# Kernel optimization log

Measured on AMD Instinct MI355X. Metric: run time of the kernel, lower is better.

The kernel has to match this reference:

```python
import jax, jax.numpy as jnp
import numpy as np

KSIZE = 3  # kernel_size from init_kwargs


def _unfold_same(x, ks):
    """Torch nn.Unfold with fixed 'same' padding. x:(B,C,H,W) -> (B, C*ks*ks, H, W).
    Channel ordering matches torch unfold: (c, kh, kw) with c outermost."""
    B, C, H, W = x.shape
    pad_total = ks - 1
    pb = pad_total // 2
    pe = pad_total - pb
    xp = jnp.pad(x, ((0, 0), (0, 0), (pb, pe), (pb, pe)))
    # small fixed loop over ks*ks = 9 taps
    patches = jnp.stack(
        [xp[:, :, di:di + H, dj:dj + W] for di in range(ks) for dj in range(ks)],
        axis=2,
    )  # (B, C, ks*ks, H, W)
    return patches.reshape(B, C * ks * ks, H, W)


def setup_inputs() -> dict:
    key = jax.random.key(0)
    k1, k2 = jax.random.split(key)
    B, C, H, W = 16, 32, 256, 256
    O, ks = 64, KSIZE
    K = C * ks * ks  # 288
    x = jax.random.normal(k1, (B, C, H, W), dtype=jnp.float32)
    limit = float(np.sqrt(6.0 / (K + O)))  # xavier_uniform
    weight = jax.random.uniform(k2, (O, K), jnp.float32, -limit, limit)
    bias = jnp.zeros((O, 1), dtype=jnp.float32)
    return {"x": x, "weight": weight, "bias": bias}


def reference(x, weight, bias):
    # Faithful math of Linear.forward: same-padded unfold, then per-pixel
    # out[n,o] = sum_k weight[o,k] * patch[n,k] + bias[o], reshaped to (B,O,H,W).
    # Expressed as a single contraction instead of the (N,O,K) broadcast intermediate.
    patches = _unfold_same(x, KSIZE)                     # (B, K, H, W)
    out = jnp.einsum('ok,bkhw->bohw', weight, patches)   # (B, O, H, W)
    out = out + bias.reshape(1, -1, 1, 1)
    return out
```

## Files before the change

kernel.cpp:

```cpp
#include <hip/hip_runtime.h>
#include <hip/hip_bf16.h>

#define CIN 32
#define OCH 64
#define HH  256
#define WW  256
#define HW  (HH * WW)
#define BH  8
#define ROWB (258 * CIN * 2)

typedef __bf16 bf16x8 __attribute__((ext_vector_type(8)));
typedef float  f32x4  __attribute__((ext_vector_type(4)));

__global__ __launch_bounds__(256, 2) void conv_fused_kernel(
        const float* __restrict__ x, const float* __restrict__ wgt,
        const float* __restrict__ bias, float* __restrict__ out) {
    const int bid = blockIdx.x;
    const int nid = (bid & 7) * 64 + (bid >> 3);
    const int b   = nid >> 5;
    const int h0  = (nid & 31) * BH;
    const int tid = threadIdx.x;
    const int l   = tid & 63, wid = tid >> 6;
    const int lm  = l & 15,  lh  = l >> 4;

    __shared__ __bf16 xs[4][258][CIN];
    char* lds = (char*)&xs[0][0][0];
    const float* xb = x + (size_t)b * CIN * HW;

    if (tid < 32) {
        const int s = tid >> 3, k = tid & 7;
        const int wp = (k < 4) ? 0 : 257;
        *(f32x4*)(lds + s * ROWB + wp * 64 + (k & 3) * 16) = (f32x4){0, 0, 0, 0};
    }

    bf16x8 af[9];
    {
        const float* wp_ = wgt + (size_t)(wid * 16 + lm) * 288 + (size_t)lh * 8 * 9;
#pragma unroll
        for (int t = 0; t < 9; ++t)
#pragma unroll
            for (int j = 0; j < 8; ++j)
                af[t][j] = (__bf16)wp_[j * 9 + t];
    }
    float bv[4];
#pragma unroll
    for (int r = 0; r < 4; ++r) bv[r] = bias[wid * 16 + lh * 4 + r];

    auto stage = [&](int row) {
        char* slot = lds + ((row + 1) & 3) * ROWB;
        if (row >= 0 && row < HH) {
            const float* rp = xb + (size_t)row * WW;
#pragma unroll
            for (int wh = 0; wh < 2; ++wh) {
                float2 v[8];
#pragma unroll
                for (int j = 0; j < 8; ++j)
                    v[j] = *(const float2*)(rp + (size_t)(wid * 8 + j) * HW + wh * 128 + 2 * l);
#pragma unroll
                for (int p = 0; p < 2; ++p) {
                    const int w = wh * 128 + 2 * l + p;
                    bf16x8 pk;
#pragma unroll
                    for (int j = 0; j < 8; ++j) pk[j] = (__bf16)(p ? v[j].y : v[j].x);
                    *(bf16x8*)(slot + (w + 1) * 64 + ((wid ^ ((w >> 1) & 3)) << 4)) = pk;
                }
            }
        } else {
#pragma unroll
            for (int wh = 0; wh < 2; ++wh)
#pragma unroll
                for (int p = 0; p < 2; ++p) {
                    const int w = wh * 128 + 2 * l + p;
                    *(f32x4*)(slot + (w + 1) * 64 + ((wid ^ ((w >> 1) & 3)) << 4)) =
                        (f32x4){0, 0, 0, 0};
                }
        }
    };

    stage(h0 - 1); stage(h0); stage(h0 + 1);

    int off[3];
#pragma unroll
    for (int kw = 0; kw < 3; ++kw) {
        const int u = lm + kw - 1;
        const int m = (u < 0) ? 3 : ((u >> 1) & 3);
        off[kw] = (lm + kw) * 64 + ((lh ^ m) << 4);
    }

    __syncthreads();

    for (int i = 0; i < BH; ++i) {
        const int h  = h0 + i;
        const int nr = h + 2;
        const bool ldnext = (i < BH - 1) && (nr < HH);
        const bool zrnext = (i < BH - 1) && (nr >= HH);

        float2 v[16];
        if (ldnext) {
            const float* rp = xb + (size_t)nr * WW;
#pragma unroll
            for (int wh = 0; wh < 2; ++wh)
#pragma unroll
                for (int j = 0; j < 8; ++j)
                    v[wh * 8 + j] =
                        *(const float2*)(rp + (size_t)(wid * 8 + j) * HW + wh * 128 + 2 * l);
        }

        const char* base[3] = { lds + ((h    ) & 3) * ROWB,
                                lds + ((h + 1) & 3) * ROWB,
                                lds + ((h + 2) & 3) * ROWB };
        f32x4 acc[16];
#pragma unroll
        for (int nt = 0; nt < 16; ++nt) acc[nt] = (f32x4){0, 0, 0, 0};
#pragma unroll
        for (int nt = 0; nt < 16; ++nt)
#pragma unroll
            for (int kh = 0; kh < 3; ++kh)
#pragma unroll
                for (int kw = 0; kw < 3; ++kw) {
                    bf16x8 bf = *(const bf16x8*)(base[kh] + off[kw] + nt * 1024);
                    acc[nt] = __builtin_amdgcn_mfma_f32_16x16x32_bf16(
                        af[kh * 3 + kw], bf, acc[nt], 0, 0, 0);
                }

        float* outb = out + (size_t)b * OCH * HW + (size_t)h * WW;
#pragma unroll
        for (int nt = 0; nt < 16; ++nt)
#pragma unroll
            for (int r2 = 0; r2 < 4; ++r2)
                outb[(size_t)(wid * 16 + lh * 4 + r2) * HW + nt * 16 + lm] =
                    acc[nt][r2] + bv[r2];

        if (ldnext) {
            char* slot = lds + ((nr + 1) & 3) * ROWB;
#pragma unroll
            for (int wh = 0; wh < 2; ++wh)
#pragma unroll
                for (int p = 0; p < 2; ++p) {
                    const int w = wh * 128 + 2 * l + p;
                    bf16x8 pk;
#pragma unroll
                    for (int j = 0; j < 8; ++j)
                        pk[j] = (__bf16)(p ? v[wh * 8 + j].y : v[wh * 8 + j].x);
                    *(bf16x8*)(slot + (w + 1) * 64 + ((wid ^ ((w >> 1) & 3)) << 4)) = pk;
                }
        } else if (zrnext) {
            char* slot = lds + ((nr + 1) & 3) * ROWB;
#pragma unroll
            for (int wh = 0; wh < 2; ++wh)
#pragma unroll
                for (int p = 0; p < 2; ++p) {
                    const int w = wh * 128 + 2 * l + p;
                    *(f32x4*)(slot + (w + 1) * 64 + ((wid ^ ((w >> 1) & 3)) << 4)) =
                        (f32x4){0, 0, 0, 0};
                }
        }
        __syncthreads();
    }
}

extern "C" void kernel_launch(void* const* d_in, const int* in_sizes, int n_in,
                              void* d_out, int out_size, void* d_ws, size_t ws_size,
                              hipStream_t stream) {
    const float* x    = (const float*)d_in[0];
    const float* w    = (const float*)d_in[1];
    const float* bias = (const float*)d_in[2];
    float* out = (float*)d_out;

    hipLaunchKernelGGL(conv_fused_kernel, dim3(16 * (HH / BH)), dim3(256), 0, stream,
                       x, w, bias, out);
}
```

Baseline: 109.3 us.

## Split warp work into 2 output groups × 8 pixel tiles to reuse LDS fragments

Each wave now computes two 16-channel output groups over half of the pixel tiles instead of one group over all tiles. Every B fragment read from LDS then feeds two MFMAs, halving LDS reads per MFMA at the cost of holding twice the weight fragments in registers. The bias is folded into the accumulator initialisation, output stores become nontemporal, and the barrier on the last iteration is dropped. The extra weight registers may pressure occupancy under the launch bound of 2 blocks.

```diff
diff --git a/kernel.cpp b/kernel.cpp
--- a/kernel.cpp
+++ b/kernel.cpp
@@ -22,6 +22,8 @@
     const int tid = threadIdx.x;
     const int l   = tid & 63, wid = tid >> 6;
     const int lm  = l & 15,  lh  = l >> 4;
+    const int ogb = (wid & 1) * 2;
+    const int ntb = (wid >> 1) * 8;
 
     __shared__ __bf16 xs[4][258][CIN];
     char* lds = (char*)&xs[0][0][0];
@@ -33,18 +35,22 @@
         *(f32x4*)(lds + s * ROWB + wp * 64 + (k & 3) * 16) = (f32x4){0, 0, 0, 0};
     }
 
-    bf16x8 af[9];
-    {
-        const float* wp_ = wgt + (size_t)(wid * 16 + lm) * 288 + (size_t)lh * 8 * 9;
+    bf16x8 af[2][9];
+#pragma unroll
+    for (int g = 0; g < 2; ++g) {
+        const float* wp_ = wgt + (size_t)((ogb + g) * 16 + lm) * 288 + (size_t)lh * 8 * 9;
 #pragma unroll
         for (int t = 0; t < 9; ++t)
 #pragma unroll
             for (int j = 0; j < 8; ++j)
-                af[t][j] = (__bf16)wp_[j * 9 + t];
+                af[g][t][j] = (__bf16)wp_[j * 9 + t];
     }
-    float bv[4];
+    float bv[2][4];
 #pragma unroll
-    for (int r = 0; r < 4; ++r) bv[r] = bias[wid * 16 + lh * 4 + r];
+    for (int g = 0; g < 2; ++g)
+#pragma unroll
+        for (int r = 0; r < 4; ++r)
+            bv[g][r] = bias[(ogb + g) * 16 + lh * 4 + r];
 
     auto stage = [&](int row) {
         char* slot = lds + ((row + 1) & 3) * ROWB;
@@ -109,27 +115,37 @@
         const char* base[3] = { lds + ((h    ) & 3) * ROWB,
                                 lds + ((h + 1) & 3) * ROWB,
                                 lds + ((h + 2) & 3) * ROWB };
-        f32x4 acc[16];
+        f32x4 acc[8][2];
 #pragma unroll
-        for (int nt = 0; nt < 16; ++nt) acc[nt] = (f32x4){0, 0, 0, 0};
+        for (int nt = 0; nt < 8; ++nt)
 #pragma unroll
-        for (int nt = 0; nt < 16; ++nt)
+            for (int g = 0; g < 2; ++g)
+                acc[nt][g] = (f32x4){bv[g][0], bv[g][1], bv[g][2], bv[g][3]};
+
+#pragma unroll
+        for (int nt = 0; nt < 8; ++nt)
 #pragma unroll
             for (int kh = 0; kh < 3; ++kh)
 #pragma unroll
                 for (int kw = 0; kw < 3; ++kw) {
-                    bf16x8 bf = *(const bf16x8*)(base[kh] + off[kw] + nt * 1024);
-                    acc[nt] = __builtin_amdgcn_mfma_f32_16x16x32_bf16(
-                        af[kh * 3 + kw], bf, acc[nt], 0, 0, 0);
+                    bf16x8 bf = *(const bf16x8*)(base[kh] + off[kw] + (ntb + nt) * 1024);
+                    acc[nt][0] = __builtin_amdgcn_mfma_f32_16x16x32_bf16(
+                        af[0][kh * 3 + kw], bf, acc[nt][0], 0, 0, 0);
+                    acc[nt][1] = __builtin_amdgcn_mfma_f32_16x16x32_bf16(
+                        af[1][kh * 3 + kw], bf, acc[nt][1], 0, 0, 0);
                 }
 
         float* outb = out + (size_t)b * OCH * HW + (size_t)h * WW;
 #pragma unroll
-        for (int nt = 0; nt < 16; ++nt)
+        for (int nt = 0; nt < 8; ++nt)
 #pragma unroll
-            for (int r2 = 0; r2 < 4; ++r2)
-                outb[(size_t)(wid * 16 + lh * 4 + r2) * HW + nt * 16 + lm] =
-                    acc[nt][r2] + bv[r2];
+            for (int g = 0; g < 2; ++g)
+#pragma unroll
+                for (int r2 = 0; r2 < 4; ++r2)
+                    __builtin_nontemporal_store(
+                        acc[nt][g][r2],
+                        &outb[(size_t)((ogb + g) * 16 + lh * 4 + r2) * HW +
+                              (ntb + nt) * 16 + lm]);
 
         if (ldnext) {
             char* slot = lds + ((nr + 1) & 3) * ROWB;
@@ -155,7 +171,7 @@
                         (f32x4){0, 0, 0, 0};
                 }
         }
-        __syncthreads();
+        if (i < BH - 1) __syncthreads();
     }
 }
 
```

Measured after the change: 156.1 us. 42.8% more time.

## Split image width across blocks with halo columns and defer output stores

Applied to the files above, without the earlier changes.

Each block now covers half the image width (128 columns plus two halo columns loaded separately), which doubles the grid to 1024 blocks, halves LDS per block, and raises the launch-bounds occupancy target from 2 to 4. The accumulator count per thread drops from 16 to 8 tiles. Bias is folded into the accumulator initialisation, and the store of each output row is deferred into the next iteration so it can overlap with the following row's loads. In exchange, every input row is loaded with extra halo-column traffic, and the single-element halo loads and stores add scattered accesses.

```diff
diff --git a/kernel.cpp b/kernel.cpp
--- a/kernel.cpp
+++ b/kernel.cpp
@@ -1,37 +1,35 @@
 #include <hip/hip_runtime.h>
 #include <hip/hip_bf16.h>
 
-#define CIN 32
-#define OCH 64
-#define HH  256
-#define WW  256
-#define HW  (HH * WW)
-#define BH  8
-#define ROWB (258 * CIN * 2)
+#define CIN  32
+#define OCH  64
+#define HH   256
+#define WW   256
+#define HW   (HH * WW)
+#define BH   8
+#define NENT 130
+#define ROWB (NENT * 64)
 
 typedef __bf16 bf16x8 __attribute__((ext_vector_type(8)));
 typedef float  f32x4  __attribute__((ext_vector_type(4)));
 
-__global__ __launch_bounds__(256, 2) void conv_fused_kernel(
+__global__ __launch_bounds__(256, 4) void conv_fused_kernel(
         const float* __restrict__ x, const float* __restrict__ wgt,
         const float* __restrict__ bias, float* __restrict__ out) {
     const int bid = blockIdx.x;
-    const int nid = (bid & 7) * 64 + (bid >> 3);
-    const int b   = nid >> 5;
-    const int h0  = (nid & 31) * BH;
+    const int nid = (bid & 7) * 128 + (bid >> 3);
+    const int wh  = nid & 1;
+    const int ht  = (nid >> 1) & 31;
+    const int b   = nid >> 6;
+    const int wbase = wh * 128;
+    const int h0    = ht * BH;
     const int tid = threadIdx.x;
     const int l   = tid & 63, wid = tid >> 6;
     const int lm  = l & 15,  lh  = l >> 4;
 
-    __shared__ __bf16 xs[4][258][CIN];
+    __shared__ __bf16 xs[4][NENT][CIN];
     char* lds = (char*)&xs[0][0][0];
     const float* xb = x + (size_t)b * CIN * HW;
-
-    if (tid < 32) {
-        const int s = tid >> 3, k = tid & 7;
-        const int wp = (k < 4) ? 0 : 257;
-        *(f32x4*)(lds + s * ROWB + wp * 64 + (k & 3) * 16) = (f32x4){0, 0, 0, 0};
-    }
 
     bf16x8 af[9];
     {
@@ -46,116 +44,131 @@
 #pragma unroll
     for (int r = 0; r < 4; ++r) bv[r] = bias[wid * 16 + lh * 4 + r];
 
-    auto stage = [&](int row) {
+    auto stageFull = [&](int row) {
         char* slot = lds + ((row + 1) & 3) * ROWB;
-        if (row >= 0 && row < HH) {
-            const float* rp = xb + (size_t)row * WW;
+        const bool rok = (row >= 0) && (row < HH);
+        const float* rp = xb + (size_t)row * WW;
+        float2 v[8];
 #pragma unroll
-            for (int wh = 0; wh < 2; ++wh) {
-                float2 v[8];
+        for (int j = 0; j < 8; ++j)
+            v[j] = rok ? *(const float2*)(rp + (size_t)(wid * 8 + j) * HW + wbase + 2 * l)
+                       : make_float2(0.f, 0.f);
 #pragma unroll
-                for (int j = 0; j < 8; ++j)
-                    v[j] = *(const float2*)(rp + (size_t)(wid * 8 + j) * HW + wh * 128 + 2 * l);
+        for (int p = 0; p < 2; ++p) {
+            const int w = wbase + 2 * l + p;
+            bf16x8 pk;
 #pragma unroll
-                for (int p = 0; p < 2; ++p) {
-                    const int w = wh * 128 + 2 * l + p;
-                    bf16x8 pk;
-#pragma unroll
-                    for (int j = 0; j < 8; ++j) pk[j] = (__bf16)(p ? v[j].y : v[j].x);
-                    *(bf16x8*)(slot + (w + 1) * 64 + ((wid ^ ((w >> 1) & 3)) << 4)) = pk;
-                }
-            }
-        } else {
-#pragma unroll
-            for (int wh = 0; wh < 2; ++wh)
-#pragma unroll
-                for (int p = 0; p < 2; ++p) {
-                    const int w = wh * 128 + 2 * l + p;
-                    *(f32x4*)(slot + (w + 1) * 64 + ((wid ^ ((w >> 1) & 3)) << 4)) =
-                        (f32x4){0, 0, 0, 0};
-                }
+            for (int j = 0; j < 8; ++j) pk[j] = (__bf16)(p ? v[j].y : v[j].x);
+            *(bf16x8*)(slot + (2 * l + p + 1) * 64 + ((wid ^ ((w >> 1) & 3)) << 4)) = pk;
+        }
+        if (tid < 64) {
+            const int side = l >> 5, ch = l & 31;
+            const int wg = wbase + (side ? 128 : -1);
+            const bool wok = rok && (wg >= 0) && (wg < WW);
+            const float hval = wok ? rp[(size_t)ch * HW + wg] : 0.f;
+            const int m = (wg < 0) ? 3 : ((wg >> 1) & 3);
+            const int e = side ? 129 : 0;
+            *(__bf16*)(slot + e * 64 + (((ch >> 3) ^ m) << 4) + (ch & 7) * 2) =
+                (__bf16)hval;
         }
     };
 
-    stage(h0 - 1); stage(h0); stage(h0 + 1);
+    stageFull(h0 - 1); stageFull(h0); stageFull(h0 + 1);
 
     int off[3];
 #pragma unroll
     for (int kw = 0; kw < 3; ++kw) {
-        const int u = lm + kw - 1;
+        const int u = wbase + lm + kw - 1;
         const int m = (u < 0) ? 3 : ((u >> 1) & 3);
         off[kw] = (lm + kw) * 64 + ((lh ^ m) << 4);
     }
 
     __syncthreads();
 
+    f32x4 acc[8];
     for (int i = 0; i < BH; ++i) {
-        const int h  = h0 + i;
+        const int h = h0 + i;
+
+        if (i > 0) {
+            float* outb = out + (size_t)b * OCH * HW + (size_t)(h - 1) * WW + wbase;
+#pragma unroll
+            for (int nt = 0; nt < 8; ++nt)
+#pragma unroll
+                for (int r2 = 0; r2 < 4; ++r2)
+                    outb[(size_t)(wid * 16 + lh * 4 + r2) * HW + nt * 16 + lm] =
+                        acc[nt][r2];
+        }
+
+#pragma unroll
+        for (int nt = 0; nt < 8; ++nt)
+            acc[nt] = (f32x4){bv[0], bv[1], bv[2], bv[3]};
+
         const int nr = h + 2;
-        const bool ldnext = (i < BH - 1) && (nr < HH);
-        const bool zrnext = (i < BH - 1) && (nr >= HH);
-
-        float2 v[16];
-        if (ldnext) {
+        const bool havenext = (i < BH - 1);
+        const bool rok2 = havenext && (nr < HH);
+        float2 v[8];
+        float hval = 0.f;
+#pragma unroll
+        for (int j = 0; j < 8; ++j) v[j] = make_float2(0.f, 0.f);
+        if (rok2) {
             const float* rp = xb + (size_t)nr * WW;
 #pragma unroll
-            for (int wh = 0; wh < 2; ++wh)
-#pragma unroll
-                for (int j = 0; j < 8; ++j)
-                    v[wh * 8 + j] =
-                        *(const float2*)(rp + (size_t)(wid * 8 + j) * HW + wh * 128 + 2 * l);
+            for (int j = 0; j < 8; ++j)
+                v[j] = *(const float2*)(rp + (size_t)(wid * 8 + j) * HW + wbase + 2 * l);
+            if (tid < 64) {
+                const int side = l >> 5;
+                const int wg = wbase + (side ? 128 : -1);
+                if (wg >= 0 && wg < WW)
+                    hval = (xb + (size_t)nr * WW)[(size_t)(l & 31) * HW + wg];
+            }
         }
 
-        const char* base[3] = { lds + ((h    ) & 3) * ROWB,
-                                lds + ((h + 1) & 3) * ROWB,
-                                lds + ((h + 2) & 3) * ROWB };
-        f32x4 acc[16];
+        const char* b0 = lds + ((h    ) & 3) * ROWB;
+        const char* b1 = lds + ((h + 1) & 3) * ROWB;
+        const char* b2 = lds + ((h + 2) & 3) * ROWB;
 #pragma unroll
-        for (int nt = 0; nt < 16; ++nt) acc[nt] = (f32x4){0, 0, 0, 0};
+        for (int nt = 0; nt < 8; ++nt) {
 #pragma unroll
-        for (int nt = 0; nt < 16; ++nt)
+            for (int kw = 0; kw < 3; ++kw) {
+                bf16x8 f0 = *(const bf16x8*)(b0 + off[kw] + nt * 1024);
+                acc[nt] = __builtin_amdgcn_mfma_f32_16x16x32_bf16(af[kw], f0, acc[nt], 0, 0, 0);
+                bf16x8 f1 = *(const bf16x8*)(b1 + off[kw] + nt * 1024);
+                acc[nt] = __builtin_amdgcn_mfma_f32_16x16x32_bf16(af[3 + kw], f1, acc[nt], 0, 0, 0);
+                bf16x8 f2 = *(const bf16x8*)(b2 + off[kw] + nt * 1024);
+                acc[nt] = __builtin_amdgcn_mfma_f32_16x16x32_bf16(af[6 + kw], f2, acc[nt], 0, 0, 0);
+            }
+        }
+
+        if (havenext) {
+            char* slot = lds + ((nr + 1) & 3) * ROWB;
 #pragma unroll
-            for (int kh = 0; kh < 3; ++kh)
+            for (int p = 0; p < 2; ++p) {
+                const int w = wbase + 2 * l + p;
+                bf16x8 pk;
 #pragma unroll
-                for (int kw = 0; kw < 3; ++kw) {
-                    bf16x8 bf = *(const bf16x8*)(base[kh] + off[kw] + nt * 1024);
-                    acc[nt] = __builtin_amdgcn_mfma_f32_16x16x32_bf16(
-                        af[kh * 3 + kw], bf, acc[nt], 0, 0, 0);
-                }
+                for (int j = 0; j < 8; ++j) pk[j] = (__bf16)(p ? v[j].y : v[j].x);
+                *(bf16x8*)(slot + (2 * l + p + 1) * 64 + ((wid ^ ((w >> 1) & 3)) << 4)) = pk;
+            }
+            if (tid < 64) {
+                const int side = l >> 5, ch = l & 31;
+                const int wg = wbase + (side ? 128 : -1);
+                const int m = (wg < 0) ? 3 : ((wg >> 1) & 3);
+                const int e = side ? 129 : 0;
+                *(__bf16*)(slot + e * 64 + (((ch >> 3) ^ m) << 4) + (ch & 7) * 2) =
+                    (__bf16)hval;
+            }
+            __syncthreads();
+        }
+    }
 
-        float* outb = out + (size_t)b * OCH * HW + (size_t)h * WW;
+    {
+        float* outb = out + (size_t)b * OCH * HW + (size_t)(h0 + BH - 1) * WW + wbase;
 #pragma unroll
-        for (int nt = 0; nt < 16; ++nt)
+        for (int nt = 0; nt < 8; ++nt)
 #pragma unroll
             for (int r2 = 0; r2 < 4; ++r2)
                 outb[(size_t)(wid * 16 + lh * 4 + r2) * HW + nt * 16 + lm] =
-                    acc[nt][r2] + bv[r2];
-
-        if (ldnext) {
-            char* slot = lds + ((nr + 1) & 3) * ROWB;
-#pragma unroll
-            for (int wh = 0; wh < 2; ++wh)
-#pragma unroll
-                for (int p = 0; p < 2; ++p) {
-                    const int w = wh * 128 + 2 * l + p;
-                    bf16x8 pk;
-#pragma unroll
-                    for (int j = 0; j < 8; ++j)
-                        pk[j] = (__bf16)(p ? v[wh * 8 + j].y : v[wh * 8 + j].x);
-                    *(bf16x8*)(slot + (w + 1) * 64 + ((wid ^ ((w >> 1) & 3)) << 4)) = pk;
-                }
-        } else if (zrnext) {
-            char* slot = lds + ((nr + 1) & 3) * ROWB;
-#pragma unroll
-            for (int wh = 0; wh < 2; ++wh)
-#pragma unroll
-                for (int p = 0; p < 2; ++p) {
-                    const int w = wh * 128 + 2 * l + p;
-                    *(f32x4*)(slot + (w + 1) * 64 + ((wid ^ ((w >> 1) & 3)) << 4)) =
-                        (f32x4){0, 0, 0, 0};
-                }
-        }
-        __syncthreads();
+                    acc[nt][r2];
     }
 }
 
@@ -167,6 +180,6 @@
     const float* bias = (const float*)d_in[2];
     float* out = (float*)d_out;
 
-    hipLaunchKernelGGL(conv_fused_kernel, dim3(16 * (HH / BH)), dim3(256), 0, stream,
+    hipLaunchKernelGGL(conv_fused_kernel, dim3(1024), dim3(256), 0, stream,
                        x, w, bias, out);
 }
```

Result: slower. 115.2 us (+5.4%).

## Switch conv MFMA tiling to 32x32x16 with 2x2 wave split

Applied to the files above, without the earlier changes.

Replaces the 16x16x32 MFMA tiling, in which each wave covered 16 output channels across all 256 pixels, with 32x32x16 MFMAs. Waves are now split two ways over output channels and two ways over pixel halves. The bias is folded into the accumulator initialisation, zero-row handling is merged into the normal store path by zero-filling the registers, and the final iteration skips its barrier. The goal is fewer LDS B-fragment reads per MFMA and fewer instructions. The cost is larger accumulator and weight register sets, with launch bounds relaxed to one block per CU minimum, which may reduce occupancy.

```diff
diff --git a/kernel.cpp b/kernel.cpp
--- a/kernel.cpp
+++ b/kernel.cpp
@@ -7,12 +7,13 @@
 #define WW  256
 #define HW  (HH * WW)
 #define BH  8
-#define ROWB (258 * CIN * 2)
+#define ROWB (258 * 64)
 
 typedef __bf16 bf16x8 __attribute__((ext_vector_type(8)));
 typedef float  f32x4  __attribute__((ext_vector_type(4)));
+typedef float  f32x16 __attribute__((ext_vector_type(16)));
 
-__global__ __launch_bounds__(256, 2) void conv_fused_kernel(
+__global__ __launch_bounds__(256, 1) void conv_fused_kernel(
         const float* __restrict__ x, const float* __restrict__ wgt,
         const float* __restrict__ bias, float* __restrict__ out) {
     const int bid = blockIdx.x;
@@ -21,7 +22,9 @@
     const int h0  = (nid & 31) * BH;
     const int tid = threadIdx.x;
     const int l   = tid & 63, wid = tid >> 6;
-    const int lm  = l & 15,  lh  = l >> 4;
+    const int lw  = l & 31,  hi  = l >> 5;
+    const int og  = wid & 1;
+    const int wf  = wid >> 1;
 
     __shared__ __bf16 xs[4][258][CIN];
     char* lds = (char*)&xs[0][0][0];
@@ -33,18 +36,21 @@
         *(f32x4*)(lds + s * ROWB + wp * 64 + (k & 3) * 16) = (f32x4){0, 0, 0, 0};
     }
 
-    bf16x8 af[9];
+    bf16x8 af[9][2];
     {
-        const float* wp_ = wgt + (size_t)(wid * 16 + lm) * 288 + (size_t)lh * 8 * 9;
+        const float* wrow = wgt + (size_t)(og * 32 + lw) * 288 + hi * 72;
 #pragma unroll
-        for (int t = 0; t < 9; ++t)
+        for (int ks = 0; ks < 2; ++ks)
 #pragma unroll
-            for (int j = 0; j < 8; ++j)
-                af[t][j] = (__bf16)wp_[j * 9 + t];
+            for (int t = 0; t < 9; ++t)
+#pragma unroll
+                for (int j = 0; j < 8; ++j)
+                    af[t][ks][j] = (__bf16)wrow[ks * 144 + j * 9 + t];
     }
-    float bv[4];
+    f32x16 bvv;
 #pragma unroll
-    for (int r = 0; r < 4; ++r) bv[r] = bias[wid * 16 + lh * 4 + r];
+    for (int r = 0; r < 16; ++r)
+        bvv[r] = bias[og * 32 + 4 * hi + (r & 3) + 8 * (r >> 2)];
 
     auto stage = [&](int row) {
         char* slot = lds + ((row + 1) & 3) * ROWB;
@@ -79,24 +85,29 @@
 
     stage(h0 - 1); stage(h0); stage(h0 + 1);
 
-    int off[3];
+    int off6[3][2];
 #pragma unroll
     for (int kw = 0; kw < 3; ++kw) {
-        const int u = lm + kw - 1;
-        const int m = (u < 0) ? 3 : ((u >> 1) & 3);
-        off[kw] = (lm + kw) * 64 + ((lh ^ m) << 4);
+        const int e = lw + kw;
+        const int m = (e == 0) ? 3 : (((e - 1) >> 1) & 3);
+#pragma unroll
+        for (int ks = 0; ks < 2; ++ks)
+            off6[kw][ks] = e * 64 + (((ks * 2 + hi) ^ m) << 4);
     }
+    const int halfoff = wf * (128 * 64);
 
     __syncthreads();
 
     for (int i = 0; i < BH; ++i) {
         const int h  = h0 + i;
         const int nr = h + 2;
-        const bool ldnext = (i < BH - 1) && (nr < HH);
-        const bool zrnext = (i < BH - 1) && (nr >= HH);
+        const bool havenext = (i < BH - 1);
+        const bool rok2 = havenext && (nr < HH);
 
         float2 v[16];
-        if (ldnext) {
+#pragma unroll
+        for (int j = 0; j < 16; ++j) v[j] = make_float2(0.f, 0.f);
+        if (rok2) {
             const float* rp = xb + (size_t)nr * WW;
 #pragma unroll
             for (int wh = 0; wh < 2; ++wh)
@@ -106,32 +117,39 @@
                         *(const float2*)(rp + (size_t)(wid * 8 + j) * HW + wh * 128 + 2 * l);
         }
 
-        const char* base[3] = { lds + ((h    ) & 3) * ROWB,
-                                lds + ((h + 1) & 3) * ROWB,
-                                lds + ((h + 2) & 3) * ROWB };
-        f32x4 acc[16];
+        const char* s0 = lds + ((h    ) & 3) * ROWB + halfoff;
+        const char* s1 = lds + ((h + 1) & 3) * ROWB + halfoff;
+        const char* s2 = lds + ((h + 2) & 3) * ROWB + halfoff;
+        f32x16 acc[4];
 #pragma unroll
-        for (int nt = 0; nt < 16; ++nt) acc[nt] = (f32x4){0, 0, 0, 0};
+        for (int t = 0; t < 4; ++t) acc[t] = bvv;
 #pragma unroll
-        for (int nt = 0; nt < 16; ++nt)
+        for (int t = 0; t < 4; ++t) {
 #pragma unroll
-            for (int kh = 0; kh < 3; ++kh)
+            for (int kh = 0; kh < 3; ++kh) {
+                const char* s = (kh == 0) ? s0 : (kh == 1) ? s1 : s2;
 #pragma unroll
-                for (int kw = 0; kw < 3; ++kw) {
-                    bf16x8 bf = *(const bf16x8*)(base[kh] + off[kw] + nt * 1024);
-                    acc[nt] = __builtin_amdgcn_mfma_f32_16x16x32_bf16(
-                        af[kh * 3 + kw], bf, acc[nt], 0, 0, 0);
-                }
+                for (int ks = 0; ks < 2; ++ks)
+#pragma unroll
+                    for (int kw = 0; kw < 3; ++kw) {
+                        bf16x8 bf = *(const bf16x8*)(s + t * 2048 + off6[kw][ks]);
+                        acc[t] = __builtin_amdgcn_mfma_f32_32x32x16_bf16(
+                            af[kh * 3 + kw][ks], bf, acc[t], 0, 0, 0);
+                    }
+            }
+        }
 
-        float* outb = out + (size_t)b * OCH * HW + (size_t)h * WW;
+        float* outb = out + ((size_t)b * OCH + og * 32 + 4 * hi) * HW +
+                      (size_t)h * WW + wf * 128 + lw;
 #pragma unroll
-        for (int nt = 0; nt < 16; ++nt)
+        for (int t = 0; t < 4; ++t)
 #pragma unroll
-            for (int r2 = 0; r2 < 4; ++r2)
-                outb[(size_t)(wid * 16 + lh * 4 + r2) * HW + nt * 16 + lm] =
-                    acc[nt][r2] + bv[r2];
+            for (int r = 0; r < 16; ++r) {
+                const int ro = (r & 3) + 8 * (r >> 2);
+                outb[(size_t)ro * HW + t * 32] = acc[t][r];
+            }
 
-        if (ldnext) {
+        if (havenext) {
             char* slot = lds + ((nr + 1) & 3) * ROWB;
 #pragma unroll
             for (int wh = 0; wh < 2; ++wh)
@@ -144,18 +162,8 @@
                         pk[j] = (__bf16)(p ? v[wh * 8 + j].y : v[wh * 8 + j].x);
                     *(bf16x8*)(slot + (w + 1) * 64 + ((wid ^ ((w >> 1) & 3)) << 4)) = pk;
                 }
-        } else if (zrnext) {
-            char* slot = lds + ((nr + 1) & 3) * ROWB;
-#pragma unroll
-            for (int wh = 0; wh < 2; ++wh)
-#pragma unroll
-                for (int p = 0; p < 2; ++p) {
-                    const int w = wh * 128 + 2 * l + p;
-                    *(f32x4*)(slot + (w + 1) * 64 + ((wid ^ ((w >> 1) & 3)) << 4)) =
-                        (f32x4){0, 0, 0, 0};
-                }
+            __syncthreads();
         }
-        __syncthreads();
     }
 }
 
@@ -167,6 +175,6 @@
     const float* bias = (const float*)d_in[2];
     float* out = (float*)d_out;
 
-    hipLaunchKernelGGL(conv_fused_kernel, dim3(16 * (HH / BH)), dim3(256), 0, stream,
+    hipLaunchKernelGGL(conv_fused_kernel, dim3(512), dim3(256), 0, stream,
                        x, w, bias, out);
 }
```

After: 115.5 us. 5.7% more time.
